# Performance work log

Measured on AMD Instinct MI355X. Metric: run time of the kernel, lower is better.

Reference implementation:

```python
import jax, jax.numpy as jnp
import numpy as np

D_MODEL = 1024
NUM_HEADS = 16
HEAD_DIM = D_MODEL // NUM_HEADS
BATCH = 2
SEQ = 2048


def setup_inputs() -> dict:
    key = jax.random.key(0)
    ks = jax.random.split(key, 9)
    s = 1.0 / np.sqrt(D_MODEL)
    inp = {
        "x": jax.random.normal(ks[0], (BATCH, SEQ, D_MODEL), dtype=jnp.float32),
        "mask": jnp.ones((BATCH, SEQ), dtype=jnp.int32),
        "Wq": jax.random.uniform(ks[1], (D_MODEL, D_MODEL), jnp.float32, -s, s),
        "bq": jax.random.uniform(ks[2], (D_MODEL,), jnp.float32, -s, s),
        "Wk": jax.random.uniform(ks[3], (D_MODEL, D_MODEL), jnp.float32, -s, s),
        "bk": jax.random.uniform(ks[4], (D_MODEL,), jnp.float32, -s, s),
        "Wv": jax.random.uniform(ks[5], (D_MODEL, D_MODEL), jnp.float32, -s, s),
        "bv": jax.random.uniform(ks[6], (D_MODEL,), jnp.float32, -s, s),
        "Wo": jax.random.uniform(ks[7], (D_MODEL, D_MODEL), jnp.float32, -s, s),
        "bo": jax.random.uniform(ks[8], (D_MODEL,), jnp.float32, -s, s),
    }
    return inp


def reference(x, mask, Wq, bq, Wk, bk, Wv, bv, Wo, bo):
    B, S, D = x.shape
    H, Hd = NUM_HEADS, HEAD_DIM
    # torch Linear: y = x @ W.T + b ; then reshape to [B, H, S, Hd]
    def proj(W, b):
        return (x @ W.T + b).reshape(B, S, H, Hd).transpose(0, 2, 1, 3)
    Q = proj(Wq, bq)
    K = proj(Wk, bk)
    V = proj(Wv, bv)
    scale = 1.0 / jnp.sqrt(jnp.asarray(Hd, dtype=x.dtype))
    scores = jnp.einsum("bhqd,bhkd->bhqk", Q, K) * scale  # [B,H,S,S]
    # mask [B,S] -> broadcast over query positions; masked_fill(mask==0, -1e9)
    scores = jnp.where(mask[:, None, None, :] == 0, jnp.asarray(-1e9, x.dtype), scores)
    attn = jax.nn.softmax(scores, axis=-1)
    context = jnp.einsum("bhqk,bhkd->bhqd", attn, V)
    context = context.transpose(0, 2, 1, 3).reshape(B, S, D)
    return context @ Wo.T + bo
```

## Files before the change

### kernel.cpp

```cpp
#include <hip/hip_runtime.h>
#include <hip/hip_bf16.h>
#include <cstdint>

#define D_MODEL 1024
#define NUM_HEADS 16
#define HEAD_DIM 64
#define BATCH 2
#define SEQ 2048
#define MROWS (BATCH * SEQ)

typedef __attribute__((ext_vector_type(8))) short bf16x8;
typedef __attribute__((ext_vector_type(4))) float f32x4;
typedef __attribute__((ext_vector_type(2))) unsigned u32x2;
typedef unsigned short u16;

#define QSCALE (0.125f * 1.44269504f)

#if __has_builtin(__builtin_amdgcn_exp2f)
#define EXP2F(x) __builtin_amdgcn_exp2f(x)
#else
#define EXP2F(x) exp2f(x)
#endif

static __device__ __forceinline__ u16 f2bf(float f) {
    unsigned int u = __float_as_uint(f);
    unsigned int lsb = (u >> 16) & 1u;
    u += 0x7fffu + lsb;
    return (u16)(u >> 16);
}

#if __has_builtin(__builtin_amdgcn_cvt_pk_bf16_f32)
static __device__ __forceinline__ unsigned pkbf(float a, float b) {
    typedef __attribute__((ext_vector_type(2))) __bf16 bf2;
    union { bf2 v; unsigned u; } cv;
    cv.v = __builtin_amdgcn_cvt_pk_bf16_f32(a, b);
    return cv.u;
}
#else
static __device__ __forceinline__ unsigned pkbf(float a, float b) {
    unsigned ua = (__float_as_uint(a) + 0x8000u) >> 16;
    unsigned ub = (__float_as_uint(b) + 0x8000u) & 0xffff0000u;
    return ua | ub;
}
#endif

#if __has_builtin(__builtin_amdgcn_permlane32_swap)
static __device__ __forceinline__ void plswap32(unsigned &a, unsigned &b) {
    u32x2 r = __builtin_amdgcn_permlane32_swap(a, b, false, false);
    a = r[0]; b = r[1];
}
#else
static __device__ __forceinline__ void plswap32(unsigned &a, unsigned &b) {
    const bool lo = ((threadIdx.x & 63) < 32);
    unsigned sa = __shfl_xor((int)a, 32, 64), sb = __shfl_xor((int)b, 32, 64);
    unsigned na = lo ? a : sb;
    unsigned nb = lo ? sa : b;
    a = na; b = nb;
}
#endif
#if __has_builtin(__builtin_amdgcn_permlane16_swap)
static __device__ __forceinline__ void plswap16(unsigned &a, unsigned &b) {
    u32x2 r = __builtin_amdgcn_permlane16_swap(a, b, false, false);
    a = r[0]; b = r[1];
}
#else
static __device__ __forceinline__ void plswap16(unsigned &a, unsigned &b) {
    const bool ev = (((threadIdx.x & 63) >> 4) & 1) == 0;
    unsigned sa = __shfl_xor((int)a, 16, 64), sb = __shfl_xor((int)b, 16, 64);
    unsigned na = ev ? a : sb;
    unsigned nb = ev ? sa : b;
    a = na; b = nb;
}
#endif

static __device__ __forceinline__ void gload_lds16(const void* g, void* l) {
    __builtin_amdgcn_global_load_lds((const __attribute__((address_space(1))) unsigned int*)g,
                                     (__attribute__((address_space(3))) unsigned int*)l,
                                     16, 0, 0);
}

__global__ void cvt_all(const float* __restrict__ x,
                        const float* __restrict__ w0, const float* __restrict__ w1,
                        const float* __restrict__ w2, const float* __restrict__ w3,
                        u16* __restrict__ base) {
    const int which = blockIdx.y;
    const int NE = D_MODEL * D_MODEL;
    const float* s;
    if (which < 4)      s = x + (size_t)which * NE;
    else if (which == 4) s = w0;
    else if (which == 5) s = w1;
    else if (which == 6) s = w2;
    else                 s = w3;
    u16* dst = base + (size_t)which * NE;
    const int i = (blockIdx.x * blockDim.x + threadIdx.x) * 4;
    float4 v = *(const float4*)(s + i);
    ushort4 o;
    o.x = f2bf(v.x); o.y = f2bf(v.y); o.z = f2bf(v.z); o.w = f2bf(v.w);
    *(ushort4*)(dst + i) = o;
}

template<int BN, int MODE>
__global__ __launch_bounds__(256, 3)
void gemm_staged(const u16* __restrict__ A, const u16* __restrict__ W,
                 const float* __restrict__ b0, const float* __restrict__ b1,
                 const float* __restrict__ b2,
                 u16* __restrict__ o0, u16* __restrict__ o1, u16* __restrict__ o2,
                 float* __restrict__ of, int K, int N) {
    constexpr int WN = BN / 2;
    constexpr int NJ = WN / 16;
    __shared__ __align__(16) u16 As[128 * 64];
    __shared__ __align__(16) u16 Bs[BN * 64];
    __shared__ __align__(16) u16 T[(MODE == 0) ? 64 * 136 : 16];

    const int lane = threadIdx.x & 63;
    const int w    = threadIdx.x >> 6;
    const int quad = lane >> 4;
    const int l16  = lane & 15;
    const int wm = w >> 1, wn = w & 1;

    const u16* Ablk = A + (size_t)(blockIdx.y * 128) * K;
    const u16* Wblk = W + (size_t)(blockIdx.x * BN) * K;

    const int srow = lane >> 3;
    const int scol = lane & 7;

    f32x4 acc[4][NJ];
#pragma unroll
    for (int i = 0; i < 4; ++i)
#pragma unroll
        for (int j = 0; j < NJ; ++j) acc[i][j] = (f32x4){0.f, 0.f, 0.f, 0.f};

    for (int kb0 = 0; kb0 < K; kb0 += 64) {
        __syncthreads();
#pragma unroll
        for (int t = 0; t < 4; ++t) {
            const int r  = w * 32 + t * 8 + srow;
            const int cg = scol ^ (r & 7);
            gload_lds16(Ablk + (size_t)r * K + kb0 + cg * 8, &As[(w * 32 + t * 8) * 64]);
        }
#pragma unroll
        for (int t = 0; t < BN / 32; ++t) {
            const int r  = w * (BN / 4) + t * 8 + srow;
            const int cg = scol ^ (r & 7);
            gload_lds16(Wblk + (size_t)r * K + kb0 + cg * 8, &Bs[(w * (BN / 4) + t * 8) * 64]);
        }
        __syncthreads();
#pragma unroll
        for (int ks = 0; ks < 2; ++ks) {
            bf16x8 a[4], b[NJ];
#pragma unroll
            for (int i = 0; i < 4; ++i) {
                const int ra = wm * 64 + 16 * i + l16;
                a[i] = *(const bf16x8*)&As[ra * 64 + ((ks * 4 + quad) ^ (ra & 7)) * 8];
            }
#pragma unroll
            for (int j = 0; j < NJ; ++j) {
                const int rb = wn * WN + 16 * j + l16;
                b[j] = *(const bf16x8*)&Bs[rb * 64 + ((ks * 4 + quad) ^ (rb & 7)) * 8];
            }
#pragma unroll
            for (int i = 0; i < 4; ++i)
#pragma unroll
                for (int j = 0; j < NJ; ++j)
                    acc[i][j] = __builtin_amdgcn_mfma_f32_16x16x32_bf16(a[i], b[j], acc[i][j], 0, 0, 0);
        }
    }

    const int mbase = blockIdx.y * 128 + wm * 64;
    const int nbase = blockIdx.x * BN + wn * WN;

    if (MODE == 0 && blockIdx.x >= 16) {
        const int mb    = blockIdx.y * 128;
        const int bb    = mb >> 11;
        const int sbase = mb & 2047;
#pragma unroll
        for (int p = 0; p < 2; ++p) {
            __syncthreads();
            if (wn == p) {
#pragma unroll
                for (int j = 0; j < NJ; ++j) {
                    const int nl = 16 * j + l16;
                    const float bv = b2[(nbase + 16 * j + l16) & 1023];
#pragma unroll
                    for (int i = 0; i < 4; ++i) {
                        const int ml = wm * 64 + 16 * i + quad * 4;
                        uint2 pk;
                        pk.x = pkbf(acc[i][j][0] + bv, acc[i][j][1] + bv);
                        pk.y = pkbf(acc[i][j][2] + bv, acc[i][j][3] + bv);
                        *(uint2*)&T[nl * 136 + ml] = pk;
                    }
                }
            }
            __syncthreads();
            const int row = threadIdx.x >> 2;
            const int gn2 = blockIdx.x * 128 + p * 64 + row;
            const int rem2 = gn2 & 1023;
            const int h = rem2 >> 6, d = rem2 & 63;
            u16* dstrow = o2 + (((size_t)(bb * NUM_HEADS + h) * 64) + d) * SEQ + sbase;
#pragma unroll
            for (int k = 0; k < 4; ++k) {
                const int chunk = (threadIdx.x & 3) * 4 + k;
                *(uint4*)(dstrow + chunk * 8) = *(const uint4*)&T[row * 136 + chunk * 8];
            }
        }
        return;
    }

    if (MODE == 0) {
#pragma unroll
        for (int j = 0; j < NJ; ++j) {
            const int gn = nbase + 16 * j + l16;
            const int which = gn >> 10, rem = gn & 1023;
            const float bv = (which == 0 ? b0 : b1)[rem];
            u16* dst = (which == 0) ? o0 : o1;
            const float scl = (which == 0) ? QSCALE : 1.0f;
            const int h = rem >> 6, d = rem & 63;
#pragma unroll
            for (int i = 0; i < 4; ++i)
#pragma unroll
                for (int r = 0; r < 4; ++r) {
                    const int gm = mbase + 16 * i + quad * 4 + r;
                    const int bb = gm >> 11, s = gm & 2047;
                    dst[(((size_t)(bb * NUM_HEADS + h) * SEQ) + s) * 64 + d] =
                        f2bf((acc[i][j][r] + bv) * scl);
                }
        }
    } else {
#pragma unroll
        for (int j = 0; j < NJ; ++j) {
            const int gn = nbase + 16 * j + l16;
            const float bv = b0[gn];
#pragma unroll
            for (int i = 0; i < 4; ++i)
#pragma unroll
                for (int r = 0; r < 4; ++r) {
                    const int gm = mbase + 16 * i + quad * 4 + r;
                    of[(size_t)gm * N + gn] = acc[i][j][r] + bv;
                }
        }
    }
}

#define SOFTMAX_PV(KBP, VIDX)                                                  \
    {                                                                          \
        if ((dirty >> (KBP)) & 1u) {                                           \
            _Pragma("unroll")                                                  \
            for (int ik = 0; ik < 4; ++ik) {                                   \
                int4 mk = *(const int4*)(mrow + (KBP) * 64 + 16 * ik + quad * 4); \
                const int* mp = (const int*)&mk;                               \
                _Pragma("unroll")                                              \
                for (int r = 0; r < 4; ++r)                                    \
                    sP[ik][r] = (mp[r] != 0) ? sP[ik][r] : -1e9f;              \
            }                                                                  \
        }                                                                      \
        float rs = 0.f;                                                        \
        unsigned c[4][2];                                                      \
        _Pragma("unroll")                                                      \
        for (int ik = 0; ik < 4; ++ik) {                                       \
            const float p0 = EXP2F(sP[ik][0]);                                 \
            const float p1 = EXP2F(sP[ik][1]);                                 \
            const float p2 = EXP2F(sP[ik][2]);                                 \
            const float p3 = EXP2F(sP[ik][3]);                                 \
            rs += (p0 + p1) + (p2 + p3);                                       \
            c[ik][0] = pkbf(p0, p1);                                           \
            c[ik][1] = pkbf(p2, p3);                                           \
        }                                                                      \
        rs += __shfl_xor(rs, 16, 64);                                          \
        rs += __shfl_xor(rs, 32, 64);                                          \
        lst += rs;                                                             \
        plswap32(c[0][0], c[1][0]); plswap32(c[0][1], c[1][1]);                \
        plswap16(c[0][0], c[1][0]); plswap16(c[0][1], c[1][1]);                \
        plswap32(c[2][0], c[3][0]); plswap32(c[2][1], c[3][1]);                \
        plswap16(c[2][0], c[3][0]); plswap16(c[2][1], c[3][1]);                \
        U u0, u1;                                                              \
        u0.d[0] = c[0][0]; u0.d[1] = c[0][1]; u0.d[2] = c[1][0]; u0.d[3] = c[1][1]; \
        u1.d[0] = c[2][0]; u1.d[1] = c[2][1]; u1.d[2] = c[3][0]; u1.d[3] = c[3][1]; \
        __builtin_amdgcn_s_setprio(1);                                         \
        _Pragma("unroll")                                                      \
        for (int ks = 0; ks < 2; ++ks) {                                       \
            const bf16x8 pf = (ks == 0) ? u0.v : u1.v;                         \
            _Pragma("unroll")                                                  \
            for (int id = 0; id < 4; ++id) {                                   \
                const int row = 16 * id + l16;                                 \
                const bf16x8 vfr = *(const bf16x8*)&Vs[VIDX][row * 64 + ((4 * ks + quad) ^ (row & 7)) * 8]; \
                o[id] = __builtin_amdgcn_mfma_f32_16x16x32_bf16(pf, vfr, o[id], 0, 0, 0); \
            }                                                                  \
        }                                                                      \
        __builtin_amdgcn_s_setprio(0);                                         \
    }

__global__ __launch_bounds__(512, 4)
void attn_kernel(const u16* __restrict__ Q, const u16* __restrict__ K,
                 const u16* __restrict__ VT, const int* __restrict__ mask,
                 u16* __restrict__ ctx) {
    __shared__ __align__(16) u16 Ks[2][64 * 64];
    __shared__ __align__(16) u16 Vs[4][64 * 64];

    const int lane = threadIdx.x & 63;
    const int w    = threadIdx.x >> 6;
    const int quad = lane >> 4;
    const int l16  = lane & 15;

    const int bh = blockIdx.x & 31;
    const int qb = blockIdx.x >> 5;
    const int b  = bh >> 4;
    const int h  = bh & 15;
    const int qbase = qb * 128 + w * 16;

    const u16* Qh = Q + (size_t)bh * SEQ * 64;
    const u16* Kh = K + (size_t)bh * SEQ * 64;
    const u16* Vh = VT + (size_t)bh * 64 * SEQ;
    const int* mrow = mask + b * SEQ;

    const int srow = lane >> 3;
    const int scol = lane & 7;
    const int cg   = scol ^ srow;

    gload_lds16(Kh + (size_t)(8 * w + srow) * 64 + cg * 8, &Ks[0][(8 * w) * 64]);
    gload_lds16(Vh + (size_t)(8 * w + srow) * SEQ + cg * 8, &Vs[0][(8 * w) * 64]);

    bf16x8 qf[2];
#pragma unroll
    for (int ks = 0; ks < 2; ++ks)
        qf[ks] = *(const bf16x8*)(Qh + (size_t)(qbase + l16) * 64 + 32 * ks + quad * 8);

    unsigned dirty = 0;
#pragma unroll
    for (int i = 0; i < 8; ++i) {
        const int4 m4 = *(const int4*)(mrow + i * 256 + lane * 4);
        const bool ok = (m4.x != 0) & (m4.y != 0) & (m4.z != 0) & (m4.w != 0);
        const unsigned long long bal = __ballot(ok);
#pragma unroll
        for (int g = 0; g < 4; ++g)
            if (((bal >> (16 * g)) & 0xffffull) != 0xffffull) dirty |= 1u << (i * 4 + g);
    }

    f32x4 o[4];
#pragma unroll
    for (int id = 0; id < 4; ++id) o[id] = (f32x4){0.f, 0.f, 0.f, 0.f};
    float lst = 0.f;
    const f32x4 fzero = (f32x4){0.f, 0.f, 0.f, 0.f};
    const int rowsel = (lane & 48) | (quad * 4);

    union U { bf16x8 v; unsigned d[4]; };
    f32x4 sP[4];

#pragma unroll 4
    for (int kb = 0; kb < 32; ++kb) {
        const int curK = kb & 1;
        __syncthreads();

        if (kb != 31) {
            const int kn = (kb + 1) * 64;
            gload_lds16(Kh + (size_t)(kn + 8 * w + srow) * 64 + cg * 8,
                        &Ks[curK ^ 1][(8 * w) * 64]);
            gload_lds16(Vh + (size_t)(8 * w + srow) * SEQ + kn + cg * 8,
                        &Vs[(kb + 1) & 3][(8 * w) * 64]);
        }

        bf16x8 kf[4][2];
#pragma unroll
        for (int ik = 0; ik < 4; ++ik) {
            const int row = 16 * ik + l16;
#pragma unroll
            for (int ks = 0; ks < 2; ++ks)
                kf[ik][ks] = *(const bf16x8*)&Ks[curK][row * 64 + ((4 * ks + quad) ^ (row & 7)) * 8];
        }

        f32x4 sN[4];
        __builtin_amdgcn_s_setprio(1);
#pragma unroll
        for (int ik = 0; ik < 4; ++ik) {
            f32x4 t = __builtin_amdgcn_mfma_f32_16x16x32_bf16(kf[ik][0], qf[0], fzero, 0, 0, 0);
            t = __builtin_amdgcn_mfma_f32_16x16x32_bf16(kf[ik][1], qf[1], t, 0, 0, 0);
            sN[ik] = t;
        }
        __builtin_amdgcn_s_setprio(0);

        if (kb > 0) SOFTMAX_PV(kb - 1, (kb - 1) & 3);

#pragma unroll
        for (int ik = 0; ik < 4; ++ik) sP[ik] = sN[ik];
    }
    SOFTMAX_PV(31, 3);

    float linv[4];
#pragma unroll
    for (int r = 0; r < 4; ++r) linv[r] = 1.f / __shfl(lst, rowsel + r, 64);
#pragma unroll
    for (int id = 0; id < 4; ++id)
#pragma unroll
        for (int r = 0; r < 4; ++r) {
            const int q = qbase + quad * 4 + r;
            const int d = 16 * id + l16;
            ctx[((size_t)(b * SEQ + q)) * D_MODEL + h * 64 + d] = f2bf(o[id][r] * linv[r]);
        }
}

extern "C" void kernel_launch(void* const* d_in, const int* in_sizes, int n_in,
                              void* d_out, int out_size, void* d_ws, size_t ws_size,
                              hipStream_t stream) {
    const float* x    = (const float*)d_in[0];
    const int*   mask = (const int*)d_in[1];
    const float* Wq   = (const float*)d_in[2];
    const float* bq   = (const float*)d_in[3];
    const float* Wk   = (const float*)d_in[4];
    const float* bk   = (const float*)d_in[5];
    const float* Wv   = (const float*)d_in[6];
    const float* bv   = (const float*)d_in[7];
    const float* Wo   = (const float*)d_in[8];
    const float* bo   = (const float*)d_in[9];

    u16* xb  = (u16*)d_ws;
    u16* wqb = xb  + (size_t)MROWS * D_MODEL;
    u16* wob = wqb + (size_t)3 * D_MODEL * D_MODEL;
    u16* Qb  = wob + (size_t)D_MODEL * D_MODEL;
    u16* Kb  = Qb  + (size_t)MROWS * D_MODEL;
    u16* VTb = Kb  + (size_t)MROWS * D_MODEL;
    u16* ctx = VTb + (size_t)MROWS * D_MODEL;

    cvt_all<<<dim3(D_MODEL * D_MODEL / 1024, 8), 256, 0, stream>>>(
        x, Wq, Wk, Wv, Wo, xb);

    gemm_staged<128, 0><<<dim3(3 * D_MODEL / 128, MROWS / 128), 256, 0, stream>>>(
        xb, wqb, bq, bk, bv, Qb, Kb, VTb, nullptr, D_MODEL, 3 * D_MODEL);

    attn_kernel<<<BATCH * NUM_HEADS * (SEQ / 128), 512, 0, stream>>>(Qb, Kb, VTb, mask, ctx);

    gemm_staged<64, 1><<<dim3(D_MODEL / 64, MROWS / 128), 256, 0, stream>>>(
        ctx, wob, bo, nullptr, nullptr, nullptr, nullptr, nullptr,
        (float*)d_out, D_MODEL, D_MODEL);
}
```

Measured before the change: 186.5 us.

## Use a three-stage K/V LDS ring with prefetch two tiles ahead

```diff
diff --git a/kernel.cpp b/kernel.cpp
--- a/kernel.cpp
+++ b/kernel.cpp
@@ -241,26 +241,52 @@
     }
 }
 
-#define SOFTMAX_PV(KBP, VIDX)                                                  \
+#define ATTN_TILE(KB, CUR)                                                     \
     {                                                                          \
-        if ((dirty >> (KBP)) & 1u) {                                           \
+        const bool clean = ((dirty >> (KB)) & 1u) == 0u;                       \
+        bf16x8 kf[4][2];                                                       \
+        _Pragma("unroll")                                                      \
+        for (int ik = 0; ik < 4; ++ik) {                                       \
+            const int row = 16 * ik + l16;                                     \
+            _Pragma("unroll")                                                  \
+            for (int ks = 0; ks < 2; ++ks)                                     \
+                kf[ik][ks] = *(const bf16x8*)&Ks[CUR][row * 64 + ((4 * ks + quad) ^ (row & 7)) * 8]; \
+        }                                                                      \
+        f32x4 s[4];                                                            \
+        __builtin_amdgcn_s_setprio(1);                                         \
+        _Pragma("unroll")                                                      \
+        for (int ik = 0; ik < 4; ++ik) {                                       \
+            f32x4 t = __builtin_amdgcn_mfma_f32_16x16x32_bf16(kf[ik][0], qf[0], fzero, 0, 0, 0); \
+            t = __builtin_amdgcn_mfma_f32_16x16x32_bf16(kf[ik][1], qf[1], t, 0, 0, 0); \
+            s[ik] = t;                                                         \
+        }                                                                      \
+        __builtin_amdgcn_s_setprio(0);                                         \
+        bf16x8 vf[4][2];                                                       \
+        _Pragma("unroll")                                                      \
+        for (int id = 0; id < 4; ++id) {                                       \
+            const int row = 16 * id + l16;                                     \
+            _Pragma("unroll")                                                  \
+            for (int ks = 0; ks < 2; ++ks)                                     \
+                vf[id][ks] = *(const bf16x8*)&Vs[CUR][row * 64 + ((4 * ks + quad) ^ (row & 7)) * 8]; \
+        }                                                                      \
+        if (!clean) {                                                          \
             _Pragma("unroll")                                                  \
             for (int ik = 0; ik < 4; ++ik) {                                   \
-                int4 mk = *(const int4*)(mrow + (KBP) * 64 + 16 * ik + quad * 4); \
+                int4 mk = *(const int4*)(mrow + (KB) * 64 + 16 * ik + quad * 4); \
                 const int* mp = (const int*)&mk;                               \
                 _Pragma("unroll")                                              \
                 for (int r = 0; r < 4; ++r)                                    \
-                    sP[ik][r] = (mp[r] != 0) ? sP[ik][r] : -1e9f;              \
+                    s[ik][r] = (mp[r] != 0) ? s[ik][r] : -1e9f;                \
             }                                                                  \
         }                                                                      \
         float rs = 0.f;                                                        \
         unsigned c[4][2];                                                      \
         _Pragma("unroll")                                                      \
         for (int ik = 0; ik < 4; ++ik) {                                       \
-            const float p0 = EXP2F(sP[ik][0]);                                 \
-            const float p1 = EXP2F(sP[ik][1]);                                 \
-            const float p2 = EXP2F(sP[ik][2]);                                 \
-            const float p3 = EXP2F(sP[ik][3]);                                 \
+            const float p0 = EXP2F(s[ik][0]);                                  \
+            const float p1 = EXP2F(s[ik][1]);                                  \
+            const float p2 = EXP2F(s[ik][2]);                                  \
+            const float p3 = EXP2F(s[ik][3]);                                  \
             rs += (p0 + p1) + (p2 + p3);                                       \
             c[ik][0] = pkbf(p0, p1);                                           \
             c[ik][1] = pkbf(p2, p3);                                           \
@@ -280,11 +306,8 @@
         for (int ks = 0; ks < 2; ++ks) {                                       \
             const bf16x8 pf = (ks == 0) ? u0.v : u1.v;                         \
             _Pragma("unroll")                                                  \
-            for (int id = 0; id < 4; ++id) {                                   \
-                const int row = 16 * id + l16;                                 \
-                const bf16x8 vfr = *(const bf16x8*)&Vs[VIDX][row * 64 + ((4 * ks + quad) ^ (row & 7)) * 8]; \
-                o[id] = __builtin_amdgcn_mfma_f32_16x16x32_bf16(pf, vfr, o[id], 0, 0, 0); \
-            }                                                                  \
+            for (int id = 0; id < 4; ++id)                                     \
+                o[id] = __builtin_amdgcn_mfma_f32_16x16x32_bf16(pf, vf[id][ks], o[id], 0, 0, 0); \
         }                                                                      \
         __builtin_amdgcn_s_setprio(0);                                         \
     }
@@ -293,8 +316,8 @@
 void attn_kernel(const u16* __restrict__ Q, const u16* __restrict__ K,
                  const u16* __restrict__ VT, const int* __restrict__ mask,
                  u16* __restrict__ ctx) {
-    __shared__ __align__(16) u16 Ks[2][64 * 64];
-    __shared__ __align__(16) u16 Vs[4][64 * 64];
+    __shared__ __align__(16) u16 Ks[3][64 * 64];
+    __shared__ __align__(16) u16 Vs[3][64 * 64];
 
     const int lane = threadIdx.x & 63;
     const int w    = threadIdx.x >> 6;
@@ -316,8 +339,10 @@
     const int scol = lane & 7;
     const int cg   = scol ^ srow;
 
-    gload_lds16(Kh + (size_t)(8 * w + srow) * 64 + cg * 8, &Ks[0][(8 * w) * 64]);
-    gload_lds16(Vh + (size_t)(8 * w + srow) * SEQ + cg * 8, &Vs[0][(8 * w) * 64]);
+    gload_lds16(Kh + (size_t)(8 * w + srow) * 64 + cg * 8,        &Ks[0][(8 * w) * 64]);
+    gload_lds16(Vh + (size_t)(8 * w + srow) * SEQ + cg * 8,       &Vs[0][(8 * w) * 64]);
+    gload_lds16(Kh + (size_t)(64 + 8 * w + srow) * 64 + cg * 8,   &Ks[1][(8 * w) * 64]);
+    gload_lds16(Vh + (size_t)(8 * w + srow) * SEQ + 64 + cg * 8,  &Vs[1][(8 * w) * 64]);
 
     bf16x8 qf[2];
 #pragma unroll
@@ -343,46 +368,27 @@
     const int rowsel = (lane & 48) | (quad * 4);
 
     union U { bf16x8 v; unsigned d[4]; };
-    f32x4 sP[4];
-
-#pragma unroll 4
-    for (int kb = 0; kb < 32; ++kb) {
-        const int curK = kb & 1;
-        __syncthreads();
-
-        if (kb != 31) {
-            const int kn = (kb + 1) * 64;
+
+#pragma unroll 3
+    for (int kb = 0; kb < 31; ++kb) {
+        const int cur = kb % 3;
+        asm volatile("s_waitcnt vmcnt(2)" ::: "memory");
+        __builtin_amdgcn_s_barrier();
+
+        if (kb < 30) {
+            const int nb = (kb + 2) % 3;
+            const int kn = (kb + 2) * 64;
             gload_lds16(Kh + (size_t)(kn + 8 * w + srow) * 64 + cg * 8,
-                        &Ks[curK ^ 1][(8 * w) * 64]);
+                        &Ks[nb][(8 * w) * 64]);
             gload_lds16(Vh + (size_t)(8 * w + srow) * SEQ + kn + cg * 8,
-                        &Vs[(kb + 1) & 3][(8 * w) * 64]);
-        }
-
-        bf16x8 kf[4][2];
-#pragma unroll
-        for (int ik = 0; ik < 4; ++ik) {
-            const int row = 16 * ik + l16;
-#pragma unroll
-            for (int ks = 0; ks < 2; ++ks)
-                kf[ik][ks] = *(const bf16x8*)&Ks[curK][row * 64 + ((4 * ks + quad) ^ (row & 7)) * 8];
-        }
-
-        f32x4 sN[4];
-        __builtin_amdgcn_s_setprio(1);
-#pragma unroll
-        for (int ik = 0; ik < 4; ++ik) {
-            f32x4 t = __builtin_amdgcn_mfma_f32_16x16x32_bf16(kf[ik][0], qf[0], fzero, 0, 0, 0);
-            t = __builtin_amdgcn_mfma_f32_16x16x32_bf16(kf[ik][1], qf[1], t, 0, 0, 0);
-            sN[ik] = t;
-        }
-        __builtin_amdgcn_s_setprio(0);
-
-        if (kb > 0) SOFTMAX_PV(kb - 1, (kb - 1) & 3);
-
-#pragma unroll
-        for (int ik = 0; ik < 4; ++ik) sP[ik] = sN[ik];
-    }
-    SOFTMAX_PV(31, 3);
+                        &Vs[nb][(8 * w) * 64]);
+        }
+
+        ATTN_TILE(kb, cur)
+    }
+    asm volatile("s_waitcnt vmcnt(0)" ::: "memory");
+    __builtin_amdgcn_s_barrier();
+    ATTN_TILE(31, 1)
 
     float linv[4];
 #pragma unroll
```

Result: slower. 199.4 us (+6.9%).
